# Kernel tuning notes

Hardware: AMD Instinct MI355X
Metric: run time of the kernel (lower is better)

## Reference

```python
import jax, jax.numpy as jnp
import numpy as np

BM = 64; BN = 64          # block_m, block_n
NKM = BM // 4; NKN = BN // 4   # tokens sampled per block (16)
# topk_newtype bands: cumulative-pooled-attention fraction -> granularity value (0 = skip block)
RATIO_BANDS = [(1, 0.05), (2, 0.15), (4, 0.25), (8, 0.5)]


def setup_inputs() -> dict:
    key = jax.random.key(0)
    kq, kk, kv, ki, kj = jax.random.split(key, 5)
    B, H, L, D = 1, 8, 4096, 64
    q = jax.random.normal(kq, (B, H, L, D), jnp.float32)
    k = jax.random.normal(kk, (B, H, L, D), jnp.float32)
    v = jax.random.normal(kv, (B, H, L, D), jnp.float32)
    # distinct in-block sample positions, shared across blocks per (B,H)
    # (mirrors torch.topk(torch.rand(B,H,1,block), sample_num))
    sample_idx_q = jnp.argsort(jax.random.uniform(ki, (B, H, BM)), axis=-1)[..., :NKM].astype(jnp.int32)
    sample_idx_k = jnp.argsort(jax.random.uniform(kj, (B, H, BN)), axis=-1)[..., :NKN].astype(jnp.int32)
    return {"q": q, "k": k, "v": v, "sample_idx_q": sample_idx_q, "sample_idx_k": sample_idx_k}


def _sample_blocks(x, idx, bs, nk):
    # x: [B,H,L,D]; idx: [B,H,nk] in-block positions -> [B,H,nb*nk,D]
    B, H, L, D = x.shape
    nb = L // bs
    xb = x.reshape(B, H, nb, bs, D)
    gidx = jnp.broadcast_to(idx[:, :, None, :, None], (B, H, nb, nk, D))
    return jnp.take_along_axis(xb, gidx, axis=3).reshape(B, H, nb * nk, D)


def _block_mask(q, k, sample_idx_q, sample_idx_k):
    # pooled downsampled attention -> per-(q_block,k_block) keep mask (topk_newtype)
    B, H, L, D = q.shape
    qb, kb = L // BM, L // BN
    sq = _sample_blocks(q, sample_idx_q, BM, NKM)  # [B,H,qb*NKM,D]
    sk = _sample_blocks(k, sample_idx_k, BN, NKN)  # [B,H,kb*NKN,D]
    scores = jnp.einsum('bhqd,bhkd->bhqk', sq, sk) / jnp.sqrt(jnp.float32(D))
    attn = jax.nn.softmax(scores, axis=-1)
    # NKM x NKN sum-pooling == block-level pooled attention mass  [B,H,qb,kb]
    pooling = attn.reshape(B, H, qb, NKM, kb, NKN).sum(axis=(3, 5))
    # rank key-blocks per q-block row by pooled mass, band by cumulative fraction
    order = jnp.argsort(-pooling, axis=-1)
    sp = jnp.take_along_axis(pooling, order, axis=-1)
    cs = jnp.cumsum(sp, axis=-1)
    frac_before = (cs - sp) / cs[..., -1:]
    val = jnp.zeros_like(sp)
    for g, hi in RATIO_BANDS[::-1]:
        val = jnp.where(frac_before < hi, jnp.float32(g), val)
    rank = jnp.argsort(order, axis=-1)          # inverse permutation
    mask_vals = jnp.take_along_axis(val, rank, axis=-1)  # [B,H,qb,kb] in {0,1,2,4,8}
    return mask_vals > 0


def reference(q, k, v, sample_idx_q, sample_idx_k):
    B, H, L, D = q.shape
    attend = _block_mask(q, k, sample_idx_q, sample_idx_k)            # [B,H,qb,kb]
    attend_tok = jnp.repeat(jnp.repeat(attend, BM, axis=2), BN, axis=3)  # [B,H,L,L]
    scores = jnp.einsum('bhqd,bhkd->bhqk', q, k) / jnp.sqrt(jnp.float32(D))
    scores = jnp.where(attend_tok, scores, jnp.float32(-1e30))
    p = jax.nn.softmax(scores, axis=-1)
    return jnp.einsum('bhqk,bhkd->bhqd', p, v)
```

## Files before the change

kernel.cpp:

```cpp
#include <hip/hip_runtime.h>
#include <hip/hip_bf16.h>

#define H_ 8
#define L_ 4096
#define D_ 64
#define NB_ 64

typedef __attribute__((ext_vector_type(8))) short bf16x8;
typedef __attribute__((ext_vector_type(4))) float f32x4;

__device__ __forceinline__ unsigned short f2bf(float x) {
    unsigned u = __float_as_uint(x);
    u += 0x7fff + ((u >> 16) & 1);
    return (unsigned short)(u >> 16);
}
__device__ __forceinline__ float bf2f(unsigned short s) {
    return __uint_as_float(((unsigned)s) << 16);
}
__device__ __forceinline__ void gload_lds16(const unsigned short* g, unsigned short* l) {
    __builtin_amdgcn_global_load_lds(
        (const __attribute__((address_space(1))) unsigned int*)(const void*)g,
        (__attribute__((address_space(3))) unsigned int*)(void*)l,
        16, 0, 0);
}

__global__ __launch_bounds__(256) void prep_kernel(
    const float* __restrict__ q, const float* __restrict__ k, const float* __restrict__ v,
    const int* __restrict__ sidxk,
    unsigned short* __restrict__ qhi, unsigned short* __restrict__ qlo,
    unsigned short* __restrict__ khi,
    unsigned short* __restrict__ vth,
    unsigned short* __restrict__ skh, unsigned short* __restrict__ skl)
{
    const int h  = blockIdx.x >> 6;
    const int tb = blockIdx.x & 63;
    const int tid = threadIdx.x;
    __shared__ float vst[64][68];

    const size_t te = ((size_t)(h*64 + tb)) << 12;
    const float4* qg = (const float4*)(q + te);
    for (int i4 = tid; i4 < 1024; i4 += 256) {
        float4 t = qg[i4];
        ushort4 hi, lo;
        hi.x = f2bf(t.x); lo.x = f2bf(t.x - bf2f(hi.x));
        hi.y = f2bf(t.y); lo.y = f2bf(t.y - bf2f(hi.y));
        hi.z = f2bf(t.z); lo.z = f2bf(t.z - bf2f(hi.z));
        hi.w = f2bf(t.w); lo.w = f2bf(t.w - bf2f(hi.w));
        *(ushort4*)(qhi + te + i4*4) = hi;
        *(ushort4*)(qlo + te + i4*4) = lo;
    }
    const float4* kg = (const float4*)(k + te);
    for (int i4 = tid; i4 < 1024; i4 += 256) {
        float4 t = kg[i4];
        int r = i4 >> 4, c4 = i4 & 15;
        int sch = (c4 >> 1) ^ ((r >> 2) & 7);
        ushort4 hi;
        hi.x = f2bf(t.x); hi.y = f2bf(t.y); hi.z = f2bf(t.z); hi.w = f2bf(t.w);
        *(ushort4*)(khi + te + r*64 + sch*8 + (c4 & 1)*4) = hi;
    }
    {
        int t = tid >> 4, d4 = tid & 15;
        int srow = tb*64 + sidxk[h*16 + t];
        float4 x = *(const float4*)(k + ((size_t)h*L_ + srow)*D_ + d4*4);
        ushort4 hi, lo;
        hi.x = f2bf(x.x); lo.x = f2bf(x.x - bf2f(hi.x));
        hi.y = f2bf(x.y); lo.y = f2bf(x.y - bf2f(hi.y));
        hi.z = f2bf(x.z); lo.z = f2bf(x.z - bf2f(hi.z));
        hi.w = f2bf(x.w); lo.w = f2bf(x.w - bf2f(hi.w));
        int sch = (d4 >> 1) ^ (t & 7);
        size_t dst = ((size_t)h*1024 + tb*16 + t)*64 + sch*8 + (d4 & 1)*4;
        *(ushort4*)(skh + dst) = hi;
        *(ushort4*)(skl + dst) = lo;
    }
    const float4* vg = (const float4*)(v + te);
    for (int i4 = tid; i4 < 1024; i4 += 256) {
        float4 t = vg[i4];
        *(float4*)&vst[i4 >> 4][(i4 & 15)*4] = t;
    }
    __syncthreads();
    for (int u = tid; u < 512; u += 256) {
        int d = u >> 3, kc8 = u & 7;
        int sch = kc8 ^ (d & 7);
        ushort4 h0, h1;
        h0.x = f2bf(vst[kc8*8+0][d]); h0.y = f2bf(vst[kc8*8+1][d]);
        h0.z = f2bf(vst[kc8*8+2][d]); h0.w = f2bf(vst[kc8*8+3][d]);
        h1.x = f2bf(vst[kc8*8+4][d]); h1.y = f2bf(vst[kc8*8+5][d]);
        h1.z = f2bf(vst[kc8*8+6][d]); h1.w = f2bf(vst[kc8*8+7][d]);
        *(ushort4*)(vth + te + d*64 + sch*8 + 0) = h0;
        *(ushort4*)(vth + te + d*64 + sch*8 + 4) = h1;
    }
}

__global__ __launch_bounds__(256, 4) void mask_mfma(
    const unsigned short* __restrict__ qhi, const unsigned short* __restrict__ qlo,
    const unsigned short* __restrict__ skh, const unsigned short* __restrict__ skl,
    const int* __restrict__ sidxq,
    unsigned long long* __restrict__ maskbits)
{
    const int h    = blockIdx.x & 7;
    const int qb   = blockIdx.x >> 3;
    const int tid  = threadIdx.x;
    const int wave = tid >> 6;
    const int lane = tid & 63;
    const int l16  = lane & 15;
    const int quad = lane >> 4;

    __shared__ __align__(16) unsigned short ch[8192];
    __shared__ __align__(16) unsigned short cl[8192];
    __shared__ float E[16][64];
    __shared__ float Z[16];
    __shared__ float pooled[64];

    for (int e = tid; e < 16*64; e += 256) (&E[0][0])[e] = 0.f;

    const int iqr = sidxq[h*16 + l16];
    const size_t qo = (((size_t)(h*64 + qb)) << 12) + (size_t)iqr*64;
    bf16x8 qh[2], ql[2];
    qh[0] = *(const bf16x8*)(qhi + qo + quad*8);
    qh[1] = *(const bf16x8*)(qhi + qo + 32 + quad*8);
    ql[0] = *(const bf16x8*)(qlo + qo + quad*8);
    ql[1] = *(const bf16x8*)(qlo + qo + 32 + quad*8);
    __syncthreads();

    for (int cc = 0; cc < 8; ++cc) {
        const bf16x8* gh = (const bf16x8*)(skh + ((size_t)h*1024 + cc*128)*64);
        const bf16x8* gl = (const bf16x8*)(skl + ((size_t)h*1024 + cc*128)*64);
        for (int i = tid; i < 1024; i += 256) {
            ((bf16x8*)ch)[i] = gh[i];
            ((bf16x8*)cl)[i] = gl[i];
        }
        __syncthreads();

        #pragma unroll
        for (int tt = 0; tt < 2; ++tt) {
            const int kb = cc*8 + wave*2 + tt;
            const int nb = (wave*2 + tt)*16;
            f32x4 sacc = (f32x4){0.f, 0.f, 0.f, 0.f};
            #pragma unroll
            for (int kc = 0; kc < 2; ++kc) {
                const int off = (nb + l16)*64 + (((kc*4 + quad) ^ (l16 & 7))*8);
                bf16x8 kh = *(const bf16x8*)&ch[off];
                bf16x8 kl = *(const bf16x8*)&cl[off];
                sacc = __builtin_amdgcn_mfma_f32_16x16x32_bf16(qh[kc], kh, sacc, 0, 0, 0);
                sacc = __builtin_amdgcn_mfma_f32_16x16x32_bf16(qh[kc], kl, sacc, 0, 0, 0);
                sacc = __builtin_amdgcn_mfma_f32_16x16x32_bf16(ql[kc], kh, sacc, 0, 0, 0);
                sacc = __builtin_amdgcn_mfma_f32_16x16x32_bf16(ql[kc], kl, sacc, 0, 0, 0);
            }
            #pragma unroll
            for (int r = 0; r < 4; ++r) {
                float p = __expf(sacc[r] * 0.125f);
                p += __shfl_xor(p, 1);
                p += __shfl_xor(p, 2);
                p += __shfl_xor(p, 4);
                p += __shfl_xor(p, 8);
                if (l16 == 0) E[quad*4 + r][kb] = p;
            }
        }
        __syncthreads();
    }

    if (tid < 16) {
        float s = 0.f;
        #pragma unroll
        for (int kb = 0; kb < 64; ++kb) s += E[tid][kb];
        Z[tid] = s;
    }
    __syncthreads();
    if (tid < 64) {
        float s = 0.f;
        #pragma unroll
        for (int t = 0; t < 16; ++t) s += E[t][tid] / Z[t];
        pooled[tid] = s;
    }
    __syncthreads();
    if (tid < 64) {
        float pi = pooled[tid];
        float tot = 0.f, bef = 0.f;
        for (int j2 = 0; j2 < 64; ++j2) {
            float pj = pooled[j2];
            tot += pj;
            if (pj > pi || (pj == pi && j2 < tid)) bef += pj;
        }
        bool att = (bef / tot) < 0.5f;
        unsigned long long bits = __ballot(att);
        if (tid == 0) maskbits[h*64 + qb] = bits;
    }
}

__global__ __launch_bounds__(256, 2) void attn_fast(
    const unsigned short* __restrict__ qhi, const unsigned short* __restrict__ qlo,
    const unsigned short* __restrict__ khi,
    const unsigned short* __restrict__ vth,
    const unsigned long long* __restrict__ maskbits,
    float* __restrict__ out)
{
    const int h    = blockIdx.x & 7;
    const int qb   = blockIdx.x >> 3;
    const int tid  = threadIdx.x;
    const int wave = tid >> 6;
    const int lane = tid & 63;
    const int l16  = lane & 15;
    const int quad = lane >> 4;

    __shared__ __align__(16) unsigned short bufK[2][4096];
    __shared__ __align__(16) unsigned short bufVh[2][4096];
    __shared__ __align__(16) unsigned short ps[4][16][88];

    const size_t qoff = (((size_t)(h*64 + qb)) << 12) + (size_t)(wave*16 + l16)*64;
    bf16x8 qfh[2], qfl[2];
    qfh[0] = *(const bf16x8*)(qhi + qoff + quad*8);
    qfh[1] = *(const bf16x8*)(qhi + qoff + 32 + quad*8);
    qfl[0] = *(const bf16x8*)(qlo + qoff + quad*8);
    qfl[1] = *(const bf16x8*)(qlo + qoff + 32 + quad*8);

    const unsigned long long bm = maskbits[(h << 6) + qb];

    float lpart[4];
    f32x4 oacc[4];
    #pragma unroll
    for (int r = 0; r < 4; ++r) lpart[r] = 0.f;
    #pragma unroll
    for (int t = 0; t < 4; ++t) oacc[t] = (f32x4){0.f, 0.f, 0.f, 0.f};

    auto dma_stage = [&](int kb, int b) {
        const size_t tb = ((size_t)(h*64 + kb)) << 12;
        gload_lds16(khi + tb + tid*8,         &bufK [b][tid*8]);
        gload_lds16(khi + tb + (tid+256)*8,   &bufK [b][(tid+256)*8]);
        gload_lds16(vth + tb + tid*8,         &bufVh[b][tid*8]);
        gload_lds16(vth + tb + (tid+256)*8,   &bufVh[b][(tid+256)*8]);
    };

    auto compute = [&](int b) {
        f32x4 sacc[4];
        #pragma unroll
        for (int t = 0; t < 4; ++t) sacc[t] = (f32x4){0.f, 0.f, 0.f, 0.f};
        #pragma unroll
        for (int t = 0; t < 4; ++t) {
            #pragma unroll
            for (int kc = 0; kc < 2; ++kc) {
                bf16x8 kf = *(const bf16x8*)&bufK[b][(l16*4 + t)*64 + (((kc*4 + quad) ^ (l16 & 7))*8)];
                sacc[t] = __builtin_amdgcn_mfma_f32_16x16x32_bf16(qfh[kc], kf, sacc[t], 0, 0, 0);
                sacc[t] = __builtin_amdgcn_mfma_f32_16x16x32_bf16(qfl[kc], kf, sacc[t], 0, 0, 0);
            }
        }
        #pragma unroll
        for (int r = 0; r < 4; ++r) {
            float p0 = __expf(fmaf(sacc[0][r], 0.125f, -16.0f));
            float p1 = __expf(fmaf(sacc[1][r], 0.125f, -16.0f));
            float p2 = __expf(fmaf(sacc[2][r], 0.125f, -16.0f));
            float p3 = __expf(fmaf(sacc[3][r], 0.125f, -16.0f));
            __hip_bfloat162 a01 = __float22bfloat162_rn(make_float2(p0, p1));
            __hip_bfloat162 a23 = __float22bfloat162_rn(make_float2(p2, p3));
            unsigned u01 = *(unsigned*)&a01;
            unsigned u23 = *(unsigned*)&a23;
            uint2 w; w.x = u01; w.y = u23;
            *(uint2*)&ps[wave][quad*4 + r][l16*4] = w;
            lpart[r] += (bf2f((unsigned short)(u01 & 0xffffu)) + bf2f((unsigned short)(u01 >> 16)))
                      + (bf2f((unsigned short)(u23 & 0xffffu)) + bf2f((unsigned short)(u23 >> 16)));
        }
        bf16x8 pf[2];
        #pragma unroll
        for (int kc = 0; kc < 2; ++kc)
            pf[kc] = *(const bf16x8*)&ps[wave][l16][kc*32 + quad*8];
        #pragma unroll
        for (int t = 0; t < 4; ++t) {
            #pragma unroll
            for (int kc = 0; kc < 2; ++kc) {
                bf16x8 vh = *(const bf16x8*)&bufVh[b][(t*16 + l16)*64 + (((kc*4 + quad) ^ (l16 & 7))*8)];
                oacc[t] = __builtin_amdgcn_mfma_f32_16x16x32_bf16(pf[kc], vh, oacc[t], 0, 0, 0);
            }
        }
    };

    unsigned long long rem = bm;
    int cur = 0;
    {
        int kb0 = (int)__builtin_ctzll(rem); rem &= rem - 1;
        dma_stage(kb0, 0);
    }
    for (;;) {
        __syncthreads();
        int nxt = -1;
        if (rem) { nxt = (int)__builtin_ctzll(rem); rem &= rem - 1; dma_stage(nxt, cur ^ 1); }
        compute(cur);
        if (nxt < 0) break;
        cur ^= 1;
    }

    #pragma unroll
    for (int off = 1; off < 16; off <<= 1)
        #pragma unroll
        for (int r = 0; r < 4; ++r)
            lpart[r] += __shfl_xor(lpart[r], off);

    float* og = out + ((size_t)h*L_ + (size_t)qb*64)*D_ + (size_t)(wave*16 + quad*4)*D_;
    #pragma unroll
    for (int r = 0; r < 4; ++r) {
        float inv = 1.f / lpart[r];
        #pragma unroll
        for (int t = 0; t < 4; ++t)
            og[(size_t)r*D_ + t*16 + l16] = oacc[t][r] * inv;
    }
}

__global__ __launch_bounds__(256, 4) void mask_kernel4(
    const float* __restrict__ q, const float* __restrict__ k,
    const int* __restrict__ sidxq, const int* __restrict__ sidxk,
    unsigned long long* __restrict__ maskbits)
{
    const int h   = blockIdx.x >> 6;
    const int qb  = blockIdx.x & 63;
    const int tid = threadIdx.x;
    const int rg  = tid >> 5;
    const int cg  = tid & 31;

    __shared__ float sq[16][68];
    __shared__ float skc[128][68];
    __shared__ float E[16][64];
    __shared__ float Z[16];
    __shared__ float pooled[64];
    __shared__ int iq[16], ik[16];

    if (tid < 16) { iq[tid] = sidxq[h*16 + tid]; ik[tid] = sidxk[h*16 + tid]; }
    for (int e = tid; e < 16*64; e += 256) (&E[0][0])[e] = 0.f;
    __syncthreads();
    {
        int j = tid >> 4, d4 = tid & 15;
        int grow = h*L_ + qb*64 + iq[j];
        *(float4*)&sq[j][d4*4] = *(const float4*)(q + (size_t)grow*D_ + d4*4);
    }
    for (int cc = 0; cc < 8; ++cc) {
        for (int i = tid; i < 2048; i += 256) {
            int col = i >> 4, d4 = i & 15;
            int colg = cc*128 + col;
            int grow = h*L_ + (colg >> 4)*64 + ik[colg & 15];
            *(float4*)&skc[col][d4*4] = *(const float4*)(k + (size_t)grow*D_ + d4*4);
        }
        __syncthreads();
        float acc[2][4] = {{0.f,0.f,0.f,0.f},{0.f,0.f,0.f,0.f}};
        #pragma unroll 4
        for (int d4 = 0; d4 < 16; ++d4) {
            float4 qv0 = *(const float4*)&sq[rg*2 + 0][d4*4];
            float4 qv1 = *(const float4*)&sq[rg*2 + 1][d4*4];
            #pragma unroll
            for (int j = 0; j < 4; ++j) {
                float4 kv = *(const float4*)&skc[cg + 32*j][d4*4];
                acc[0][j] += qv0.x*kv.x + qv0.y*kv.y + qv0.z*kv.z + qv0.w*kv.w;
                acc[1][j] += qv1.x*kv.x + qv1.y*kv.y + qv1.z*kv.z + qv1.w*kv.w;
            }
        }
        #pragma unroll
        for (int j = 0; j < 4; ++j) {
            int kb = cc*8 + (cg >> 4) + 2*j;
            #pragma unroll
            for (int i = 0; i < 2; ++i) {
                float p = __expf(acc[i][j] * 0.125f);
                p += __shfl_xor(p, 1);
                p += __shfl_xor(p, 2);
                p += __shfl_xor(p, 4);
                p += __shfl_xor(p, 8);
                if ((cg & 15) == 0) E[rg*2 + i][kb] += p;
            }
        }
        __syncthreads();
    }
    if (tid < 16) {
        float s = 0.f;
        #pragma unroll
        for (int kb = 0; kb < 64; ++kb) s += E[tid][kb];
        Z[tid] = s;
    }
    __syncthreads();
    if (tid < 64) {
        float s = 0.f;
        #pragma unroll
        for (int t = 0; t < 16; ++t) s += E[t][tid] / Z[t];
        pooled[tid] = s;
    }
    __syncthreads();
    if (tid < 64) {
        float pi = pooled[tid];
        float tot = 0.f, bef = 0.f;
        for (int j2 = 0; j2 < 64; ++j2) {
            float pj = pooled[j2];
            tot += pj;
            if (pj > pi || (pj == pi && j2 < tid)) bef += pj;
        }
        bool att = (bef / tot) < 0.5f;
        unsigned long long bits = __ballot(att);
        if (tid == 0) maskbits[h*64 + qb] = bits;
    }
}

__global__ __launch_bounds__(256, 3) void attn_v3(
    const float* __restrict__ q, const float* __restrict__ k, const float* __restrict__ v,
    const unsigned long long* __restrict__ maskbits, float* __restrict__ out)
{
    const int h = blockIdx.x >> 6, qb = blockIdx.x & 63;
    const int tid = threadIdx.x, wave = tid >> 6, lane = tid & 63;
    const int l16 = lane & 15, quad = lane >> 4;
    __shared__ __align__(16) unsigned short ks_hi[64][72];
    __shared__ __align__(16) unsigned short ks_lo[64][72];
    __shared__ __align__(16) unsigned short vt_hi[64][72];
    __shared__ __align__(16) unsigned short vt_lo[64][72];
    __shared__ __align__(16) unsigned short ps[4][16][72];

    const float4* qg = (const float4*)(q + ((size_t)h*L_ + (size_t)qb*64)*D_);
    for (int i4 = tid; i4 < 1024; i4 += 256) {
        float4 t = qg[i4];
        int r = i4 >> 4, c = (i4 & 15) << 2;
        ushort4 hi, lo;
        hi.x = f2bf(t.x); lo.x = f2bf(t.x - bf2f(hi.x));
        hi.y = f2bf(t.y); lo.y = f2bf(t.y - bf2f(hi.y));
        hi.z = f2bf(t.z); lo.z = f2bf(t.z - bf2f(hi.z));
        hi.w = f2bf(t.w); lo.w = f2bf(t.w - bf2f(hi.w));
        *(ushort4*)&ks_hi[r][c] = hi;
        *(ushort4*)&ks_lo[r][c] = lo;
    }
    const unsigned long long bm = maskbits[(h << 6) + qb];
    __syncthreads();
    bf16x8 qhi2[2], qlo2[2];
    #pragma unroll
    for (int kc = 0; kc < 2; ++kc) {
        qhi2[kc] = *(const bf16x8*)&ks_hi[wave*16 + l16][kc*32 + quad*8];
        qlo2[kc] = *(const bf16x8*)&ks_lo[wave*16 + l16][kc*32 + quad*8];
    }
    __syncthreads();
    float m_i[4], l_i[4];
    f32x4 oacc[4];
    #pragma unroll
    for (int r = 0; r < 4; ++r) { m_i[r] = -1e30f; l_i[r] = 0.f; }
    #pragma unroll
    for (int t = 0; t < 4; ++t) oacc[t] = (f32x4){0.f, 0.f, 0.f, 0.f};
    for (int kb = 0; kb < 64; ++kb) {
        if (!((bm >> kb) & 1ull)) continue;
        const float4* kg = (const float4*)(k + ((size_t)h*L_ + (size_t)kb*64)*D_);
        const float*  vg = v + ((size_t)h*L_ + (size_t)kb*64)*D_;
        for (int i4 = tid; i4 < 1024; i4 += 256) {
            float4 t = kg[i4];
            int r = i4 >> 4, c = (i4 & 15) << 2;
            ushort4 hi, lo;
            hi.x = f2bf(t.x); lo.x = f2bf(t.x - bf2f(hi.x));
            hi.y = f2bf(t.y); lo.y = f2bf(t.y - bf2f(hi.y));
            hi.z = f2bf(t.z); lo.z = f2bf(t.z - bf2f(hi.z));
            hi.w = f2bf(t.w); lo.w = f2bf(t.w - bf2f(hi.w));
            *(ushort4*)&ks_hi[r][c] = hi;
            *(ushort4*)&ks_lo[r][c] = lo;
        }
        for (int tsk = tid; tsk < 512; tsk += 256) {
            int rp = tsk >> 4;
            int c  = (tsk & 15) << 2;
            float4 a0 = *(const float4*)(vg + (size_t)(2*rp)*D_ + c);
            float4 a1 = *(const float4*)(vg + (size_t)(2*rp+1)*D_ + c);
            #pragma unroll
            for (int j = 0; j < 4; ++j) {
                float x0 = (j==0)?a0.x:(j==1)?a0.y:(j==2)?a0.z:a0.w;
                float x1 = (j==0)?a1.x:(j==1)?a1.y:(j==2)?a1.z:a1.w;
                unsigned short h0 = f2bf(x0), h1b = f2bf(x1);
                *(unsigned*)&vt_hi[c+j][2*rp] = (unsigned)h0 | ((unsigned)h1b << 16);
                unsigned short lo0 = f2bf(x0 - bf2f(h0)), lo1 = f2bf(x1 - bf2f(h1b));
                *(unsigned*)&vt_lo[c+j][2*rp] = (unsigned)lo0 | ((unsigned)lo1 << 16);
            }
        }
        __syncthreads();
        f32x4 sacc[4];
        #pragma unroll
        for (int t = 0; t < 4; ++t) sacc[t] = (f32x4){0.f, 0.f, 0.f, 0.f};
        #pragma unroll
        for (int t = 0; t < 4; ++t) {
            #pragma unroll
            for (int kc = 0; kc < 2; ++kc) {
                bf16x8 khi2 = *(const bf16x8*)&ks_hi[t*16 + l16][kc*32 + quad*8];
                bf16x8 klo2 = *(const bf16x8*)&ks_lo[t*16 + l16][kc*32 + quad*8];
                sacc[t] = __builtin_amdgcn_mfma_f32_16x16x32_bf16(qhi2[kc], khi2, sacc[t], 0, 0, 0);
                sacc[t] = __builtin_amdgcn_mfma_f32_16x16x32_bf16(qhi2[kc], klo2, sacc[t], 0, 0, 0);
                sacc[t] = __builtin_amdgcn_mfma_f32_16x16x32_bf16(qlo2[kc], khi2, sacc[t], 0, 0, 0);
            }
        }
        #pragma unroll
        for (int t = 0; t < 4; ++t) sacc[t] *= 0.125f;
        float rowmax[4];
        #pragma unroll
        for (int r = 0; r < 4; ++r)
            rowmax[r] = fmaxf(fmaxf(sacc[0][r], sacc[1][r]), fmaxf(sacc[2][r], sacc[3][r]));
        #pragma unroll
        for (int off = 1; off < 16; off <<= 1)
            #pragma unroll
            for (int r = 0; r < 4; ++r)
                rowmax[r] = fmaxf(rowmax[r], __shfl_xor(rowmax[r], off));
        float al[4], rs[4];
        #pragma unroll
        for (int r = 0; r < 4; ++r) {
            float mnew = fmaxf(m_i[r], rowmax[r]);
            al[r] = __expf(m_i[r] - mnew);
            m_i[r] = mnew;
            float acc = 0.f;
            #pragma unroll
            for (int t = 0; t < 4; ++t) {
                float p = __expf(sacc[t][r] - mnew);
                unsigned short pb = f2bf(p);
                ps[wave][quad*4 + r][t*16 + l16] = pb;
                acc += bf2f(pb);
            }
            rs[r] = acc;
        }
        #pragma unroll
        for (int off = 1; off < 16; off <<= 1)
            #pragma unroll
            for (int r = 0; r < 4; ++r)
                rs[r] += __shfl_xor(rs[r], off);
        #pragma unroll
        for (int r = 0; r < 4; ++r) l_i[r] = l_i[r] * al[r] + rs[r];
        #pragma unroll
        for (int t = 0; t < 4; ++t)
            #pragma unroll
            for (int r = 0; r < 4; ++r) oacc[t][r] *= al[r];
        bf16x8 pf[2];
        #pragma unroll
        for (int kc = 0; kc < 2; ++kc)
            pf[kc] = *(const bf16x8*)&ps[wave][l16][kc*32 + quad*8];
        #pragma unroll
        for (int t = 0; t < 4; ++t) {
            #pragma unroll
            for (int kc = 0; kc < 2; ++kc) {
                bf16x8 vhif = *(const bf16x8*)&vt_hi[t*16 + l16][kc*32 + quad*8];
                bf16x8 vlof = *(const bf16x8*)&vt_lo[t*16 + l16][kc*32 + quad*8];
                oacc[t] = __builtin_amdgcn_mfma_f32_16x16x32_bf16(pf[kc], vhif, oacc[t], 0, 0, 0);
                oacc[t] = __builtin_amdgcn_mfma_f32_16x16x32_bf16(pf[kc], vlof, oacc[t], 0, 0, 0);
            }
        }
        __syncthreads();
    }
    float* og = out + ((size_t)h*L_ + (size_t)qb*64)*D_ + (size_t)(wave*16 + quad*4)*D_;
    #pragma unroll
    for (int r = 0; r < 4; ++r) {
        float inv = 1.f / l_i[r];
        #pragma unroll
        for (int t = 0; t < 4; ++t)
            og[(size_t)r*D_ + t*16 + l16] = oacc[t][r] * inv;
    }
}

extern "C" void kernel_launch(void* const* d_in, const int* in_sizes, int n_in,
                              void* d_out, int out_size, void* d_ws, size_t ws_size,
                              hipStream_t stream) {
    const float* q = (const float*)d_in[0];
    const float* k = (const float*)d_in[1];
    const float* v = (const float*)d_in[2];
    const int* siq = (const int*)d_in[3];
    const int* sik = (const int*)d_in[4];
    float* out = (float*)d_out;

    char* ws = (char*)d_ws;
    unsigned long long* mask = (unsigned long long*)ws;
    const size_t TEN = (size_t)H_*L_*D_;
    const size_t SKN = (size_t)H_*1024*64;
    unsigned short* qhi = (unsigned short*)(ws + 4096);
    unsigned short* qlo = qhi + TEN;
    unsigned short* khi = qlo + TEN;
    unsigned short* vth = khi + TEN;
    unsigned short* skh = vth + TEN;
    unsigned short* skl = skh + SKN;
    const size_t need = 4096 + (4*TEN + 2*SKN)*sizeof(unsigned short);

    if (ws_size >= need) {
        prep_kernel<<<dim3(H_*NB_), dim3(256), 0, stream>>>(q, k, v, sik, qhi, qlo, khi, vth, skh, skl);
        mask_mfma<<<dim3(H_*NB_), dim3(256), 0, stream>>>(qhi, qlo, skh, skl, siq, mask);
        attn_fast<<<dim3(H_*NB_), dim3(256), 0, stream>>>(qhi, qlo, khi, vth, mask, out);
    } else {
        mask_kernel4<<<dim3(H_*NB_), dim3(256), 0, stream>>>(q, k, siq, sik, mask);
        attn_v3<<<dim3(H_*NB_), dim3(256), 0, stream>>>(q, k, v, mask, out);
    }
}
```

Measured before the change: 147.1 us.

## Split attention key blocks across two workgroups and add combine kernel

The attention kernel now launches twice as many workgroups, and each handles alternating kept key blocks of a query block. Each one writes unnormalized partial outputs and row sums to workspace, and a new combine kernel adds the halves and normalizes. The aim is more parallelism and better CU occupancy, since the previous 512-workgroup grid underfilled the GPU. The cost is an extra launch plus about 16MB of extra global traffic. The row-sum accumulation also now uses the fp32 probabilities rather than the bf16-rounded ones.

```diff
diff --git a/kernel.cpp b/kernel.cpp
--- a/kernel.cpp
+++ b/kernel.cpp
@@ -187,15 +187,17 @@
     }
 }
 
-__global__ __launch_bounds__(256, 2) void attn_fast(
+__global__ __launch_bounds__(256, 3) void attn_split(
     const unsigned short* __restrict__ qhi, const unsigned short* __restrict__ qlo,
     const unsigned short* __restrict__ khi,
     const unsigned short* __restrict__ vth,
     const unsigned long long* __restrict__ maskbits,
-    float* __restrict__ out)
+    float* __restrict__ outp,
+    float* __restrict__ lp)
 {
     const int h    = blockIdx.x & 7;
-    const int qb   = blockIdx.x >> 3;
+    const int qb   = (blockIdx.x >> 3) & 63;
+    const int s    = blockIdx.x >> 9;
     const int tid  = threadIdx.x;
     const int wave = tid >> 6;
     const int lane = tid & 63;
@@ -214,6 +216,15 @@
     qfl[1] = *(const bf16x8*)(qlo + qoff + 32 + quad*8);
 
     const unsigned long long bm = maskbits[(h << 6) + qb];
+    unsigned long long mine = 0ull;
+    {
+        unsigned long long t = bm; int i = 0;
+        while (t) {
+            unsigned long long lb = t & (0ull - t);
+            if ((i & 1) == s) mine |= lb;
+            t ^= lb; ++i;
+        }
+    }
 
     float lpart[4];
     f32x4 oacc[4];
@@ -251,12 +262,9 @@
             float p3 = __expf(fmaf(sacc[3][r], 0.125f, -16.0f));
             __hip_bfloat162 a01 = __float22bfloat162_rn(make_float2(p0, p1));
             __hip_bfloat162 a23 = __float22bfloat162_rn(make_float2(p2, p3));
-            unsigned u01 = *(unsigned*)&a01;
-            unsigned u23 = *(unsigned*)&a23;
-            uint2 w; w.x = u01; w.y = u23;
+            uint2 w; w.x = *(unsigned*)&a01; w.y = *(unsigned*)&a23;
             *(uint2*)&ps[wave][quad*4 + r][l16*4] = w;
-            lpart[r] += (bf2f((unsigned short)(u01 & 0xffffu)) + bf2f((unsigned short)(u01 >> 16)))
-                      + (bf2f((unsigned short)(u23 & 0xffffu)) + bf2f((unsigned short)(u23 >> 16)));
+            lpart[r] += (p0 + p1) + (p2 + p3);
         }
         bf16x8 pf[2];
         #pragma unroll
@@ -272,19 +280,21 @@
         }
     };
 
-    unsigned long long rem = bm;
-    int cur = 0;
-    {
-        int kb0 = (int)__builtin_ctzll(rem); rem &= rem - 1;
-        dma_stage(kb0, 0);
-    }
-    for (;;) {
-        __syncthreads();
-        int nxt = -1;
-        if (rem) { nxt = (int)__builtin_ctzll(rem); rem &= rem - 1; dma_stage(nxt, cur ^ 1); }
-        compute(cur);
-        if (nxt < 0) break;
-        cur ^= 1;
+    if (mine) {
+        unsigned long long rem = mine;
+        int cur = 0;
+        {
+            int kb0 = (int)__builtin_ctzll(rem); rem &= rem - 1;
+            dma_stage(kb0, 0);
+        }
+        for (;;) {
+            __syncthreads();
+            int nxt = -1;
+            if (rem) { nxt = (int)__builtin_ctzll(rem); rem &= rem - 1; dma_stage(nxt, cur ^ 1); }
+            compute(cur);
+            if (nxt < 0) break;
+            cur ^= 1;
+        }
     }
 
     #pragma unroll
@@ -293,14 +303,31 @@
         for (int r = 0; r < 4; ++r)
             lpart[r] += __shfl_xor(lpart[r], off);
 
-    float* og = out + ((size_t)h*L_ + (size_t)qb*64)*D_ + (size_t)(wave*16 + quad*4)*D_;
+    float* og = outp + (size_t)s*(H_*L_*D_)
+              + ((size_t)h*L_ + qb*64 + wave*16 + quad*4)*D_;
     #pragma unroll
     for (int r = 0; r < 4; ++r) {
-        float inv = 1.f / lpart[r];
         #pragma unroll
         for (int t = 0; t < 4; ++t)
-            og[(size_t)r*D_ + t*16 + l16] = oacc[t][r] * inv;
-    }
+            og[(size_t)r*D_ + t*16 + l16] = oacc[t][r];
+        if (l16 == 0)
+            lp[(size_t)s*(H_*L_) + (size_t)h*L_ + qb*64 + wave*16 + quad*4 + r] = lpart[r];
+    }
+}
+
+__global__ __launch_bounds__(256) void combine_kernel(
+    const float* __restrict__ outp, const float* __restrict__ lp,
+    float* __restrict__ out)
+{
+    const int idx4 = blockIdx.x * 256 + threadIdx.x;
+    const int row  = idx4 >> 4;
+    float inv = 1.f / (lp[row] + lp[(size_t)(H_*L_) + row]);
+    float4 a = *(const float4*)(outp + (size_t)idx4*4);
+    float4 b = *(const float4*)(outp + (size_t)(H_*L_*D_) + (size_t)idx4*4);
+    float4 o;
+    o.x = (a.x + b.x) * inv; o.y = (a.y + b.y) * inv;
+    o.z = (a.z + b.z) * inv; o.w = (a.w + b.w) * inv;
+    *(float4*)(out + (size_t)idx4*4) = o;
 }
 
 __global__ __launch_bounds__(256, 4) void mask_kernel4(
@@ -561,12 +588,16 @@
     unsigned short* vth = khi + TEN;
     unsigned short* skh = vth + TEN;
     unsigned short* skl = skh + SKN;
-    const size_t need = 4096 + (4*TEN + 2*SKN)*sizeof(unsigned short);
+    float* outp = (float*)(skl + SKN);
+    float* lp   = outp + 2*TEN;
+    const size_t need = 4096 + (4*TEN + 2*SKN)*sizeof(unsigned short)
+                      + (2*TEN + 2*(size_t)H_*L_)*sizeof(float);
 
     if (ws_size >= need) {
         prep_kernel<<<dim3(H_*NB_), dim3(256), 0, stream>>>(q, k, v, sik, qhi, qlo, khi, vth, skh, skl);
         mask_mfma<<<dim3(H_*NB_), dim3(256), 0, stream>>>(qhi, qlo, skh, skl, siq, mask);
-        attn_fast<<<dim3(H_*NB_), dim3(256), 0, stream>>>(qhi, qlo, khi, vth, mask, out);
+        attn_split<<<dim3(2*H_*NB_), dim3(256), 0, stream>>>(qhi, qlo, khi, vth, mask, outp, lp);
+        combine_kernel<<<dim3(2048), dim3(256), 0, stream>>>(outp, lp, out);
     } else {
         mask_kernel4<<<dim3(H_*NB_), dim3(256), 0, stream>>>(q, k, siq, sik, mask);
         attn_v3<<<dim3(H_*NB_), dim3(256), 0, stream>>>(q, k, v, mask, out);
```

Measured after the change: 152.0 us. 3.3% more time.
